# Kernel optimization log

Measured on AMD Instinct MI355X. Metric: run time of the kernel, lower is better.

Reference implementation:

```python
import jax, jax.numpy as jnp
import numpy as np


def _relative_position_index(wd, wh, ww):
    coords = np.stack(np.meshgrid(np.arange(wd), np.arange(wh), np.arange(ww), indexing='ij'))
    flat = coords.reshape(3, -1)                      # (3, N)
    rel = flat[:, :, None] - flat[:, None, :]         # (3, N, N)
    rel = rel.transpose(1, 2, 0).astype(np.int64)     # (N, N, 3)
    rel[..., 0] += wd - 1
    rel[..., 1] += wh - 1
    rel[..., 2] += ww - 1
    rel[..., 0] *= (2 * wh - 1) * (2 * ww - 1)
    rel[..., 1] *= (2 * ww - 1)
    return rel.sum(-1)                                 # (N, N)


def setup_inputs() -> dict:
    key = jax.random.key(0)
    k0, k1, k2, k3 = jax.random.split(key, 4)
    B, D, H, W = 4, 16, 56, 56
    wd, wh, ww = 8, 7, 7
    C, nH = 128, 4
    N = wd * wh * ww                                   # 392
    nW = (D // wd) * (H // wh) * (W // ww)             # 128
    B_ = B * nW                                        # 512
    table_sz = (2 * wd - 1) * (2 * wh - 1) * (2 * ww - 1)  # 2535
    x = jax.random.normal(k0, (B_, N, C), jnp.float32)
    mask = jnp.zeros((nW, N, N), jnp.float32)          # 0/-inf additive mask; zeros = no shift
    qkv_w = jax.random.normal(k1, (3 * C, C), jnp.float32) * 0.02
    proj_w = jax.random.normal(k2, (C, C), jnp.float32) * 0.02
    proj_b = jnp.zeros((C,), jnp.float32)
    bias_table = jax.random.normal(k3, (table_sz, nH), jnp.float32) * 0.02
    rel_index = jnp.asarray(_relative_position_index(wd, wh, ww), jnp.int32)
    return {"x": x, "mask": mask, "qkv_w": qkv_w, "proj_w": proj_w,
            "proj_b": proj_b, "bias_table": bias_table, "rel_index": rel_index}


def reference(x, mask, qkv_w, proj_w, proj_b, bias_table, rel_index):
    B_, N, C = x.shape
    nH = bias_table.shape[1]
    hd = C // nH
    scale = hd ** -0.5
    # qkv projection (no bias, qkv_bias=False)
    qkv = (x @ qkv_w.T).reshape(B_, N, 3, nH, hd).transpose(2, 0, 3, 1, 4)  # (3,B_,H,N,hd)
    q, k, v = qkv[0] * scale, qkv[1], qkv[2]
    attn = jnp.einsum('bhnd,bhmd->bhnm', q, k)                              # (B_,H,N,N)
    bias = bias_table[rel_index.reshape(-1)].reshape(N, N, nH).transpose(2, 0, 1)
    attn = attn + bias[None]
    nW = mask.shape[0]
    attn = attn.reshape(B_ // nW, nW, nH, N, N) + mask[None, :, None]
    attn = jax.nn.softmax(attn.reshape(B_, nH, N, N), axis=-1)
    out = jnp.einsum('bhnm,bhmd->bhnd', attn, v)                            # (B_,H,N,hd)
    out = out.transpose(0, 2, 1, 3).reshape(B_, N, C)
    return out @ proj_w.T + proj_b
```

## Files before the change

kernel.cpp:

```cpp
#include <hip/hip_runtime.h>

typedef unsigned short u16;
typedef unsigned int   u32;

#define NTOK   392
#define NN2    153664
#define LOG2E  1.44269504088896340736f
#define QSCL   (0.17677669529663687f * 1.44269504088896340736f)
#define BTQ    416
#define BTH    (416L*416L)

typedef __attribute__((ext_vector_type(8))) __bf16 bf16x8;
typedef __attribute__((ext_vector_type(4))) float  f32x4;
#define MFMA16(a,b,c) __builtin_amdgcn_mfma_f32_16x16x32_bf16((a),(b),(c),0,0,0)

__device__ __forceinline__ float bf2f(u16 u){
    union { u32 i; float f; } v; v.i = ((u32)u) << 16; return v.f;
}
__device__ __forceinline__ u16 f2bf(float x){
    union { float f; u32 i; } v; v.f = x;
    u32 r = (v.i + 0x7FFFu + ((v.i >> 16) & 1u)) >> 16;
    return (u16)r;
}
__device__ __forceinline__ u16 bfbits(float x){
    union { __bf16 b; u16 u; } v; v.b = (__bf16)x; return v.u;
}
__device__ __forceinline__ float ldf(const void* p, int isb, long i){
    if (isb) return bf2f(((const u16*)p)[i]);
    else     return ((const float*)p)[i];
}
__device__ __forceinline__ void stf(void* p, int isb, long i, float v){
    if (isb) ((u16*)p)[i] = f2bf(v);
    else     ((float*)p)[i] = v;
}

__device__ __forceinline__ void ld8s(const void* p, int isb, long i0,
                                     bf16x8* h, bf16x8* l){
    union { u16 u[8]; bf16x8 v; } H, L;
    if (isb){
        const uint2* q = (const uint2*)((const u16*)p + i0);
        uint2 a = q[0], b = q[1];
        H.u[0]=(u16)a.x; H.u[1]=(u16)(a.x>>16); H.u[2]=(u16)a.y; H.u[3]=(u16)(a.y>>16);
        H.u[4]=(u16)b.x; H.u[5]=(u16)(b.x>>16); H.u[6]=(u16)b.y; H.u[7]=(u16)(b.y>>16);
        #pragma unroll
        for (int j = 0; j < 8; ++j) L.u[j] = 0;
    } else {
        const float4* q = (const float4*)((const float*)p + i0);
        float4 a = q[0], b = q[1];
        float f[8] = {a.x,a.y,a.z,a.w,b.x,b.y,b.z,b.w};
        #pragma unroll
        for (int j = 0; j < 8; ++j){
            u16 hh = f2bf(f[j]);
            H.u[j] = hh;
            L.u[j] = f2bf(f[j] - bf2f(hh));
        }
    }
    *h = H.v; *l = L.v;
}

__device__ __forceinline__ int plaus(u16 w){
    int e = (w >> 7) & 0xFF;
    return (w == 0) || (e >= 96 && e <= 145);
}
__global__ __launch_bounds__(256) void prep_kernel(
        const u16* __restrict__ x, int* __restrict__ flags){
    __shared__ int cnt[2];
    int tid = threadIdx.x;
    if (tid < 2) cnt[tid] = 0;
    __syncthreads();
    int p = plaus(x[tid]) + plaus(x[tid + 256]);
    if (p) atomicAdd(&cnt[0], p);
    int ez = ((tid & 1) == 0 && x[tid] == 0) + (((tid + 256) & 1) == 0 && x[tid + 256] == 0);
    if (ez) atomicAdd(&cnt[1], ez);
    __syncthreads();
    if (tid == 0){
        flags[0] = (cnt[1] < 64 && cnt[0] >= 436) ? 1 : 0;
        flags[4] = 0;
    }
}

__global__ __launch_bounds__(256) void mask_scan_kernel(
        const u32* __restrict__ m, int nhalf, const int* __restrict__ flagsRO,
        int* __restrict__ flags){
    long nw = flagsRO[0] ? nhalf : 2L * nhalf;
    long i0 = (long)blockIdx.x * 256 + threadIdx.x;
    u32 acc = 0;
    for (long i = i0; i < nw; i += (long)gridDim.x * 256) acc |= m[i];
    if (acc) atomicOr(&flags[4], 1);
}

__global__ __launch_bounds__(256) void bias_expand_kernel(
        const int* __restrict__ rel_index, const void* btabP,
        const int* __restrict__ flags, float* __restrict__ biasT){
    long idx = (long)blockIdx.x * 256 + threadIdx.x;
    if (idx >= BTH) return;
    int key = (int)(idx / BTQ);
    int q   = (int)(idx - (long)key * BTQ);
    int isb = flags[0];
    float v0, v1, v2, v3;
    if (key >= NTOK){ v0 = v1 = v2 = v3 = -1e30f; }
    else if (q >= NTOK){ v0 = v1 = v2 = v3 = 0.f; }
    else {
        int t = rel_index[(long)q * NTOK + key];
        v0 = ldf(btabP, isb, (long)t * 4 + 0) * LOG2E;
        v1 = ldf(btabP, isb, (long)t * 4 + 1) * LOG2E;
        v2 = ldf(btabP, isb, (long)t * 4 + 2) * LOG2E;
        v3 = ldf(btabP, isb, (long)t * 4 + 3) * LOG2E;
    }
    biasT[0 * BTH + idx] = v0;
    biasT[1 * BTH + idx] = v1;
    biasT[2 * BTH + idx] = v2;
    biasT[3 * BTH + idx] = v3;
}

__global__ __launch_bounds__(512) void attn_mfma_kernel(
        const void* xP, const void* qwP, const void* maskP,
        const float* __restrict__ biasT, const int* __restrict__ flags,
        void* outP){
    __shared__ __align__(16) u16 Qh[416 * 40];
    __shared__ __align__(16) u16 Kh[416 * 40];
    __shared__ __align__(16) u16 VT[32 * 424];
    __shared__ __align__(16) u16 uni[2 * 64 * 136];

    u16* xs_hi = uni;
    u16* xs_lo = uni + 64 * 136;

    const int tid  = threadIdx.x;
    const int lane = tid & 63;
    const int wv   = tid >> 6;
    const int c    = lane & 15;
    const int g    = lane >> 4;
    const int h    = blockIdx.y;
    const int b_   = blockIdx.x;
    const int wdx  = b_ & 127;
    const int isb  = flags[0], fm = flags[4];
    const long xbase = (long)b_ * NTOK * 128;

    for (int i = tid; i < 24 * 40; i += 512){ Qh[392 * 40 + i] = 0; Kh[392 * 40 + i] = 0; }
    for (int i = tid; i < 32 * 32; i += 512) VT[(i >> 5) * 424 + 392 + (i & 31)] = 0;

    const int mt  = wv >> 1;
    const int ntb = (wv & 1) * 3;
    bf16x8 WH[3][4], WL[3][4];
    #pragma unroll
    for (int j = 0; j < 3; ++j){
        int n = (ntb + j) * 16 + c;
        int wrow = (n < 32) ? (h * 32 + n)
                 : (n < 64) ? (128 + h * 32 + (n - 32))
                 :            (256 + h * 32 + (n - 64));
        #pragma unroll
        for (int ks = 0; ks < 4; ++ks)
            ld8s(qwP, isb, (long)wrow * 128 + ks * 32 + 8 * g, &WH[j][ks], &WL[j][ks]);
    }

    for (int ch = 0; ch < 7; ++ch){
        const int tok0 = ch * 64;
        __syncthreads();
        #pragma unroll
        for (int jj = 0; jj < 4; ++jj){
            int idx = jj * 2048 + tid * 4;
            int r = idx >> 7, cc = idx & 127;
            int row = tok0 + r;
            u32 h01, h23, l01, l23;
            if (row < NTOK){
                long gi = xbase + (long)row * 128 + cc;
                if (isb){
                    uint2 a = *(const uint2*)((const u16*)xP + gi);
                    h01 = a.x; h23 = a.y; l01 = 0; l23 = 0;
                } else {
                    float4 f = *(const float4*)((const float*)xP + gi);
                    u16 h0=f2bf(f.x), h1=f2bf(f.y), h2=f2bf(f.z), h3=f2bf(f.w);
                    h01 = h0 | ((u32)h1 << 16); h23 = h2 | ((u32)h3 << 16);
                    l01 = (u32)f2bf(f.x - bf2f(h0)) | ((u32)f2bf(f.y - bf2f(h1)) << 16);
                    l23 = (u32)f2bf(f.z - bf2f(h2)) | ((u32)f2bf(f.w - bf2f(h3)) << 16);
                }
            } else { h01 = h23 = l01 = l23 = 0; }
            *(uint2*)&xs_hi[r * 136 + cc] = make_uint2(h01, h23);
            *(uint2*)&xs_lo[r * 136 + cc] = make_uint2(l01, l23);
        }
        __syncthreads();
        #pragma unroll
        for (int j = 0; j < 3; ++j){
            f32x4 acc = {0.f, 0.f, 0.f, 0.f};
            #pragma unroll
            for (int ks = 0; ks < 4; ++ks){
                bf16x8 ah = *(const bf16x8*)&xs_hi[(mt * 16 + c) * 136 + ks * 32 + 8 * g];
                bf16x8 al = *(const bf16x8*)&xs_lo[(mt * 16 + c) * 136 + ks * 32 + 8 * g];
                acc = MFMA16(ah, WH[j][ks], acc);
                acc = MFMA16(al, WH[j][ks], acc);
                acc = MFMA16(ah, WL[j][ks], acc);
            }
            int n = (ntb + j) * 16 + c;
            #pragma unroll
            for (int i = 0; i < 4; ++i){
                int tok = tok0 + mt * 16 + 4 * g + i;
                if (tok < NTOK){
                    if (n < 32)      Qh[tok * 40 + n]         = f2bf(acc[i] * QSCL);
                    else if (n < 64) Kh[tok * 40 + (n - 32)]  = f2bf(acc[i]);
                    else             VT[(n - 64) * 424 + tok] = f2bf(acc[i]);
                }
            }
        }
    }
    __syncthreads();

    u16* pbA = uni + wv * 1280;
    u16* pbB = pbA + 640;
    const float* bT = biasT + (long)h * BTH;
    const long mb = (long)wdx * NN2;

    for (int task = wv; task < 13; task += 8){
        const int qa0 = task * 32;
        const int qb0 = qa0 + 16;
        bf16x8 qA = *(const bf16x8*)&Qh[(qa0 + c) * 40 + 8 * g];
        bf16x8 qB = *(const bf16x8*)&Qh[(qb0 + c) * 40 + 8 * g];
        f32x4 oA0={0.f,0.f,0.f,0.f}, oA1={0.f,0.f,0.f,0.f};
        f32x4 oB0={0.f,0.f,0.f,0.f}, oB1={0.f,0.f,0.f,0.f};
        float rsA0=0.f,rsA1=0.f,rsA2=0.f,rsA3=0.f;
        float rsB0=0.f,rsB1=0.f,rsB2=0.f,rsB3=0.f;
        const float* bp = bT + (long)c * BTQ + qa0 + 4 * g;
        f32x4 rA0 = *(const f32x4*)(bp);
        f32x4 rB0 = *(const f32x4*)(bp + 16);
        f32x4 rA1 = *(const f32x4*)(bp + 16 * BTQ);
        f32x4 rB1 = *(const f32x4*)(bp + 16 * BTQ + 16);
        const float* fp = bp + 32 * BTQ;

        for (int k2 = 0; k2 < 13; ++k2){
            {
                const int kt = 2 * k2;
                bf16x8 kb = *(const bf16x8*)&Kh[(kt * 16 + c) * 40 + 8 * g];
                f32x4 cA = rA0, cB = rB0;
                if (k2 < 12){
                    rA0 = *(const f32x4*)(fp);
                    rB0 = *(const f32x4*)(fp + 16);
                }
                if (fm){
                    int key = kt * 16 + c; int kc = key < NTOK ? key : NTOK - 1;
                    #pragma unroll
                    for (int i = 0; i < 4; ++i){
                        int qa_ = qa0 + 4 * g + i; if (qa_ >= NTOK) qa_ = NTOK - 1;
                        int qb_ = qb0 + 4 * g + i; if (qb_ >= NTOK) qb_ = NTOK - 1;
                        cA[i] += ldf(maskP, isb, mb + (long)qa_ * NTOK + kc) * LOG2E;
                        cB[i] += ldf(maskP, isb, mb + (long)qb_ * NTOK + kc) * LOG2E;
                    }
                }
                f32x4 sA = MFMA16(qA, kb, cA);
                f32x4 sB = MFMA16(qB, kb, cB);
                float pA[4], pB[4];
                #pragma unroll
                for (int i = 0; i < 4; ++i){ pA[i] = exp2f(sA[i]); pB[i] = exp2f(sB[i]); }
                rsA0 += pA[0]; rsA1 += pA[1]; rsA2 += pA[2]; rsA3 += pA[3];
                rsB0 += pB[0]; rsB1 += pB[1]; rsB2 += pB[2]; rsB3 += pB[3];
                #pragma unroll
                for (int i = 0; i < 4; ++i){
                    pbA[(4 * g + i) * 40 + c] = bfbits(pA[i]);
                    pbB[(4 * g + i) * 40 + c] = bfbits(pB[i]);
                }
            }
            {
                const int kt = 2 * k2 + 1;
                bf16x8 kb = *(const bf16x8*)&Kh[(kt * 16 + c) * 40 + 8 * g];
                f32x4 cA = rA1, cB = rB1;
                if (k2 < 12){
                    rA1 = *(const f32x4*)(fp + 16 * BTQ);
                    rB1 = *(const f32x4*)(fp + 16 * BTQ + 16);
                    fp += 32 * BTQ;
                }
                if (fm){
                    int key = kt * 16 + c; int kc = key < NTOK ? key : NTOK - 1;
                    #pragma unroll
                    for (int i = 0; i < 4; ++i){
                        int qa_ = qa0 + 4 * g + i; if (qa_ >= NTOK) qa_ = NTOK - 1;
                        int qb_ = qb0 + 4 * g + i; if (qb_ >= NTOK) qb_ = NTOK - 1;
                        cA[i] += ldf(maskP, isb, mb + (long)qa_ * NTOK + kc) * LOG2E;
                        cB[i] += ldf(maskP, isb, mb + (long)qb_ * NTOK + kc) * LOG2E;
                    }
                }
                f32x4 sA = MFMA16(qA, kb, cA);
                f32x4 sB = MFMA16(qB, kb, cB);
                float pA[4], pB[4];
                #pragma unroll
                for (int i = 0; i < 4; ++i){ pA[i] = exp2f(sA[i]); pB[i] = exp2f(sB[i]); }
                rsA0 += pA[0]; rsA1 += pA[1]; rsA2 += pA[2]; rsA3 += pA[3];
                rsB0 += pB[0]; rsB1 += pB[1]; rsB2 += pB[2]; rsB3 += pB[3];
                #pragma unroll
                for (int i = 0; i < 4; ++i){
                    pbA[(4 * g + i) * 40 + 16 + c] = bfbits(pA[i]);
                    pbB[(4 * g + i) * 40 + 16 + c] = bfbits(pB[i]);
                }
                bf16x8 paA = *(const bf16x8*)&pbA[c * 40 + 8 * g];
                bf16x8 paB = *(const bf16x8*)&pbB[c * 40 + 8 * g];
                int kk = k2 * 32 + 8 * g;
                bf16x8 v0 = *(const bf16x8*)&VT[c * 424 + kk];
                bf16x8 v1 = *(const bf16x8*)&VT[(c + 16) * 424 + kk];
                oA0 = MFMA16(paA, v0, oA0);
                oA1 = MFMA16(paA, v1, oA1);
                oB0 = MFMA16(paB, v0, oB0);
                oB1 = MFMA16(paB, v1, oB1);
            }
        }
        float rsA[4] = {rsA0, rsA1, rsA2, rsA3};
        float rsB[4] = {rsB0, rsB1, rsB2, rsB3};
        #pragma unroll
        for (int m = 1; m < 16; m <<= 1){
            #pragma unroll
            for (int i = 0; i < 4; ++i){
                rsA[i] += __shfl_xor(rsA[i], m, 64);
                rsB[i] += __shfl_xor(rsB[i], m, 64);
            }
        }
        #pragma unroll
        for (int i = 0; i < 4; ++i){
            int ta = qa0 + 4 * g + i;
            if (ta < NTOK){
                float ia = 1.f / rsA[i];
                stf(outP, isb, xbase + (long)ta * 128 + h * 32 + c,      oA0[i] * ia);
                stf(outP, isb, xbase + (long)ta * 128 + h * 32 + 16 + c, oA1[i] * ia);
            }
            int tb = qb0 + 4 * g + i;
            if (tb < NTOK){
                float ib = 1.f / rsB[i];
                stf(outP, isb, xbase + (long)tb * 128 + h * 32 + c,      oB0[i] * ib);
                stf(outP, isb, xbase + (long)tb * 128 + h * 32 + 16 + c, oB1[i] * ib);
            }
        }
    }
}

__global__ __launch_bounds__(512) void proj_mfma_kernel(
        const void* wP, const void* bP, const int* __restrict__ flags,
        void* outP){
    __shared__ __align__(16) u16 xs_hi[64 * 136];
    __shared__ __align__(16) u16 xs_lo[64 * 136];
    const int tid  = threadIdx.x;
    const int lane = tid & 63;
    const int wv   = tid >> 6;
    const int c    = lane & 15;
    const int g    = lane >> 4;
    const int isb  = flags[0];
    const long m0  = (long)blockIdx.x * 64;

    #pragma unroll
    for (int jj = 0; jj < 4; ++jj){
        int idx = jj * 2048 + tid * 4;
        int r = idx >> 7, cc = idx & 127;
        long gi = (m0 + r) * 128 + cc;
        u32 h01, h23, l01, l23;
        if (isb){
            uint2 a = *(const uint2*)((const u16*)outP + gi);
            h01 = a.x; h23 = a.y; l01 = 0; l23 = 0;
        } else {
            float4 f = *(const float4*)((const float*)outP + gi);
            u16 h0=f2bf(f.x), h1=f2bf(f.y), h2=f2bf(f.z), h3=f2bf(f.w);
            h01 = h0 | ((u32)h1 << 16); h23 = h2 | ((u32)h3 << 16);
            l01 = (u32)f2bf(f.x - bf2f(h0)) | ((u32)f2bf(f.y - bf2f(h1)) << 16);
            l23 = (u32)f2bf(f.z - bf2f(h2)) | ((u32)f2bf(f.w - bf2f(h3)) << 16);
        }
        *(uint2*)&xs_hi[r * 136 + cc] = make_uint2(h01, h23);
        *(uint2*)&xs_lo[r * 136 + cc] = make_uint2(l01, l23);
    }
    __syncthreads();
    const int mt  = wv >> 1;
    const int ntb = (wv & 1) * 4;
    bf16x8 ah[4], al[4];
    #pragma unroll
    for (int ks = 0; ks < 4; ++ks){
        ah[ks] = *(const bf16x8*)&xs_hi[(mt * 16 + c) * 136 + ks * 32 + 8 * g];
        al[ks] = *(const bf16x8*)&xs_lo[(mt * 16 + c) * 136 + ks * 32 + 8 * g];
    }
    #pragma unroll
    for (int j = 0; j < 4; ++j){
        int nt = ntb + j;
        bf16x8 wh[4], wl[4];
        #pragma unroll
        for (int ks = 0; ks < 4; ++ks)
            ld8s(wP, isb, (long)(nt * 16 + c) * 128 + ks * 32 + 8 * g, &wh[ks], &wl[ks]);
        f32x4 acc = {0.f,0.f,0.f,0.f};
        #pragma unroll
        for (int ks = 0; ks < 4; ++ks){
            acc = MFMA16(ah[ks], wh[ks], acc);
            acc = MFMA16(al[ks], wh[ks], acc);
            acc = MFMA16(ah[ks], wl[ks], acc);
        }
        float bias = ldf(bP, isb, nt * 16 + c);
        #pragma unroll
        for (int i = 0; i < 4; ++i){
            long row = m0 + mt * 16 + 4 * g + i;
            stf(outP, isb, row * 128 + nt * 16 + c, acc[i] + bias);
        }
    }
}

extern "C" void kernel_launch(void* const* d_in, const int* in_sizes, int n_in,
                              void* d_out, int out_size, void* d_ws, size_t ws_size,
                              hipStream_t stream){
    const void* x      = d_in[0];
    const void* mask   = d_in[1];
    const void* qkv_w  = d_in[2];
    const void* proj_w = d_in[3];
    const void* proj_b = d_in[4];
    const void* btab   = d_in[5];
    const int*  relidx = (const int*)d_in[6];

    int*   flags = (int*)d_ws;
    float* biasT = (float*)((char*)d_ws + 256);

    prep_kernel<<<dim3(1), dim3(256), 0, stream>>>((const u16*)x, flags);
    int nhalf = in_sizes[1] / 2;
    mask_scan_kernel<<<dim3(2048), dim3(256), 0, stream>>>(
        (const u32*)mask, nhalf, flags, flags);
    bias_expand_kernel<<<dim3((int)((BTH + 255) / 256)), dim3(256), 0, stream>>>(
        relidx, btab, flags, biasT);
    attn_mfma_kernel<<<dim3(512, 4), dim3(512), 0, stream>>>(
        x, qkv_w, mask, biasT, flags, d_out);
    proj_mfma_kernel<<<dim3(3136), dim3(512), 0, stream>>>(
        proj_w, proj_b, flags, d_out);
}
```

Before: 719.8 us.

## Use 13 waves per attention block with transposed score MFMA and bias layout

```diff
diff --git a/kernel.cpp b/kernel.cpp
--- a/kernel.cpp
+++ b/kernel.cpp
@@ -7,7 +7,7 @@
 #define NN2    153664
 #define LOG2E  1.44269504088896340736f
 #define QSCL   (0.17677669529663687f * 1.44269504088896340736f)
-#define BTQ    416
+#define BTK    416
 #define BTH    (416L*416L)
 
 typedef __attribute__((ext_vector_type(8))) __bf16 bf16x8;
@@ -24,6 +24,9 @@
 }
 __device__ __forceinline__ u16 bfbits(float x){
     union { __bf16 b; u16 u; } v; v.b = (__bf16)x; return v.u;
+}
+__device__ __forceinline__ u32 pk2(float a, float b){
+    return (u32)bfbits(a) | ((u32)bfbits(b) << 16);
 }
 __device__ __forceinline__ float ldf(const void* p, int isb, long i){
     if (isb) return bf2f(((const u16*)p)[i]);
@@ -91,11 +94,11 @@
 
 __global__ __launch_bounds__(256) void bias_expand_kernel(
         const int* __restrict__ rel_index, const void* btabP,
-        const int* __restrict__ flags, float* __restrict__ biasT){
+        const int* __restrict__ flags, float* __restrict__ biasF){
     long idx = (long)blockIdx.x * 256 + threadIdx.x;
     if (idx >= BTH) return;
-    int key = (int)(idx / BTQ);
-    int q   = (int)(idx - (long)key * BTQ);
+    int q   = (int)(idx / BTK);
+    int key = (int)(idx - (long)q * BTK);
     int isb = flags[0];
     float v0, v1, v2, v3;
     if (key >= NTOK){ v0 = v1 = v2 = v3 = -1e30f; }
@@ -107,15 +110,15 @@
         v2 = ldf(btabP, isb, (long)t * 4 + 2) * LOG2E;
         v3 = ldf(btabP, isb, (long)t * 4 + 3) * LOG2E;
     }
-    biasT[0 * BTH + idx] = v0;
-    biasT[1 * BTH + idx] = v1;
-    biasT[2 * BTH + idx] = v2;
-    biasT[3 * BTH + idx] = v3;
-}
-
-__global__ __launch_bounds__(512) void attn_mfma_kernel(
+    biasF[0 * BTH + idx] = v0;
+    biasF[1 * BTH + idx] = v1;
+    biasF[2 * BTH + idx] = v2;
+    biasF[3 * BTH + idx] = v3;
+}
+
+__global__ __launch_bounds__(832) void attn_mfma_kernel(
         const void* xP, const void* qwP, const void* maskP,
-        const float* __restrict__ biasT, const int* __restrict__ flags,
+        const float* __restrict__ biasF, const int* __restrict__ flags,
         void* outP){
     __shared__ __align__(16) u16 Qh[416 * 40];
     __shared__ __align__(16) u16 Kh[416 * 40];
@@ -136,64 +139,71 @@
     const int isb  = flags[0], fm = flags[4];
     const long xbase = (long)b_ * NTOK * 128;
 
-    for (int i = tid; i < 24 * 40; i += 512){ Qh[392 * 40 + i] = 0; Kh[392 * 40 + i] = 0; }
-    for (int i = tid; i < 32 * 32; i += 512) VT[(i >> 5) * 424 + 392 + (i & 31)] = 0;
-
-    const int mt  = wv >> 1;
-    const int ntb = (wv & 1) * 3;
-    bf16x8 WH[3][4], WL[3][4];
-    #pragma unroll
-    for (int j = 0; j < 3; ++j){
-        int n = (ntb + j) * 16 + c;
-        int wrow = (n < 32) ? (h * 32 + n)
-                 : (n < 64) ? (128 + h * 32 + (n - 32))
-                 :            (256 + h * 32 + (n - 64));
-        #pragma unroll
-        for (int ks = 0; ks < 4; ++ks)
-            ld8s(qwP, isb, (long)wrow * 128 + ks * 32 + 8 * g, &WH[j][ks], &WL[j][ks]);
+    for (int i = tid; i < 24 * 40; i += 832){ Qh[392 * 40 + i] = 0; Kh[392 * 40 + i] = 0; }
+    for (int i = tid; i < 32 * 32; i += 832) VT[(i >> 5) * 424 + 392 + (i & 31)] = 0;
+
+    const int nt0 = wv >> 2,        mt0 = wv & 3;
+    const int nt1 = (wv + 13) >> 2, mt1 = (wv + 13) & 3;
+    const int has1 = (wv < 11);
+    bf16x8 W0h[4], W0l[4], W1h[4], W1l[4];
+    {
+        int n0 = nt0 * 16 + c;
+        int wr0 = (n0 < 32) ? (h * 32 + n0)
+                : (n0 < 64) ? (128 + h * 32 + (n0 - 32))
+                :             (256 + h * 32 + (n0 - 64));
+        int n1 = nt1 * 16 + c;
+        int wr1 = (n1 < 32) ? (h * 32 + n1)
+                : (n1 < 64) ? (128 + h * 32 + (n1 - 32))
+                :             (256 + h * 32 + (n1 - 64));
+        #pragma unroll
+        for (int ks = 0; ks < 4; ++ks){
+            ld8s(qwP, isb, (long)wr0 * 128 + ks * 32 + 8 * g, &W0h[ks], &W0l[ks]);
+            if (has1)
+                ld8s(qwP, isb, (long)wr1 * 128 + ks * 32 + 8 * g, &W1h[ks], &W1l[ks]);
+        }
     }
 
     for (int ch = 0; ch < 7; ++ch){
         const int tok0 = ch * 64;
         __syncthreads();
-        #pragma unroll
-        for (int jj = 0; jj < 4; ++jj){
-            int idx = jj * 2048 + tid * 4;
+        for (int idx = tid * 4; idx < 8192; idx += 3328){
             int r = idx >> 7, cc = idx & 127;
             int row = tok0 + r;
-            u32 h01, h23, l01, l23;
-            if (row < NTOK){
-                long gi = xbase + (long)row * 128 + cc;
-                if (isb){
-                    uint2 a = *(const uint2*)((const u16*)xP + gi);
-                    h01 = a.x; h23 = a.y; l01 = 0; l23 = 0;
-                } else {
-                    float4 f = *(const float4*)((const float*)xP + gi);
+            if (isb){
+                uint2 a = make_uint2(0u, 0u);
+                if (row < NTOK)
+                    a = *(const uint2*)((const u16*)xP + xbase + (long)row * 128 + cc);
+                *(uint2*)&xs_hi[r * 136 + cc] = a;
+            } else {
+                u32 h01, h23, l01, l23;
+                if (row < NTOK){
+                    float4 f = *(const float4*)((const float*)xP + xbase + (long)row * 128 + cc);
                     u16 h0=f2bf(f.x), h1=f2bf(f.y), h2=f2bf(f.z), h3=f2bf(f.w);
                     h01 = h0 | ((u32)h1 << 16); h23 = h2 | ((u32)h3 << 16);
                     l01 = (u32)f2bf(f.x - bf2f(h0)) | ((u32)f2bf(f.y - bf2f(h1)) << 16);
                     l23 = (u32)f2bf(f.z - bf2f(h2)) | ((u32)f2bf(f.w - bf2f(h3)) << 16);
-                }
-            } else { h01 = h23 = l01 = l23 = 0; }
-            *(uint2*)&xs_hi[r * 136 + cc] = make_uint2(h01, h23);
-            *(uint2*)&xs_lo[r * 136 + cc] = make_uint2(l01, l23);
+                } else { h01 = h23 = l01 = l23 = 0; }
+                *(uint2*)&xs_hi[r * 136 + cc] = make_uint2(h01, h23);
+                *(uint2*)&xs_lo[r * 136 + cc] = make_uint2(l01, l23);
+            }
         }
         __syncthreads();
-        #pragma unroll
-        for (int j = 0; j < 3; ++j){
+        {
             f32x4 acc = {0.f, 0.f, 0.f, 0.f};
             #pragma unroll
             for (int ks = 0; ks < 4; ++ks){
-                bf16x8 ah = *(const bf16x8*)&xs_hi[(mt * 16 + c) * 136 + ks * 32 + 8 * g];
-                bf16x8 al = *(const bf16x8*)&xs_lo[(mt * 16 + c) * 136 + ks * 32 + 8 * g];
-                acc = MFMA16(ah, WH[j][ks], acc);
-                acc = MFMA16(al, WH[j][ks], acc);
-                acc = MFMA16(ah, WL[j][ks], acc);
-            }
-            int n = (ntb + j) * 16 + c;
+                bf16x8 ah = *(const bf16x8*)&xs_hi[(mt0 * 16 + c) * 136 + ks * 32 + 8 * g];
+                acc = MFMA16(ah, W0h[ks], acc);
+                if (!isb){
+                    bf16x8 al = *(const bf16x8*)&xs_lo[(mt0 * 16 + c) * 136 + ks * 32 + 8 * g];
+                    acc = MFMA16(al, W0h[ks], acc);
+                    acc = MFMA16(ah, W0l[ks], acc);
+                }
+            }
+            int n = nt0 * 16 + c;
             #pragma unroll
             for (int i = 0; i < 4; ++i){
-                int tok = tok0 + mt * 16 + 4 * g + i;
+                int tok = tok0 + mt0 * 16 + 4 * g + i;
                 if (tok < NTOK){
                     if (n < 32)      Qh[tok * 40 + n]         = f2bf(acc[i] * QSCL);
                     else if (n < 64) Kh[tok * 40 + (n - 32)]  = f2bf(acc[i]);
@@ -201,128 +211,115 @@
                 }
             }
         }
+        if (has1){
+            f32x4 acc = {0.f, 0.f, 0.f, 0.f};
+            #pragma unroll
+            for (int ks = 0; ks < 4; ++ks){
+                bf16x8 ah = *(const bf16x8*)&xs_hi[(mt1 * 16 + c) * 136 + ks * 32 + 8 * g];
+                acc = MFMA16(ah, W1h[ks], acc);
+                if (!isb){
+                    bf16x8 al = *(const bf16x8*)&xs_lo[(mt1 * 16 + c) * 136 + ks * 32 + 8 * g];
+                    acc = MFMA16(al, W1h[ks], acc);
+                    acc = MFMA16(ah, W1l[ks], acc);
+                }
+            }
+            int n = nt1 * 16 + c;
+            #pragma unroll
+            for (int i = 0; i < 4; ++i){
+                int tok = tok0 + mt1 * 16 + 4 * g + i;
+                if (tok < NTOK){
+                    if (n < 32)      Qh[tok * 40 + n]         = f2bf(acc[i] * QSCL);
+                    else if (n < 64) Kh[tok * 40 + (n - 32)]  = f2bf(acc[i]);
+                    else             VT[(n - 64) * 424 + tok] = f2bf(acc[i]);
+                }
+            }
+        }
     }
     __syncthreads();
 
     u16* pbA = uni + wv * 1280;
     u16* pbB = pbA + 640;
-    const float* bT = biasT + (long)h * BTH;
-    const long mb = (long)wdx * NN2;
-
-    for (int task = wv; task < 13; task += 8){
-        const int qa0 = task * 32;
-        const int qb0 = qa0 + 16;
-        bf16x8 qA = *(const bf16x8*)&Qh[(qa0 + c) * 40 + 8 * g];
-        bf16x8 qB = *(const bf16x8*)&Qh[(qb0 + c) * 40 + 8 * g];
-        f32x4 oA0={0.f,0.f,0.f,0.f}, oA1={0.f,0.f,0.f,0.f};
-        f32x4 oB0={0.f,0.f,0.f,0.f}, oB1={0.f,0.f,0.f,0.f};
-        float rsA0=0.f,rsA1=0.f,rsA2=0.f,rsA3=0.f;
-        float rsB0=0.f,rsB1=0.f,rsB2=0.f,rsB3=0.f;
-        const float* bp = bT + (long)c * BTQ + qa0 + 4 * g;
-        f32x4 rA0 = *(const f32x4*)(bp);
-        f32x4 rB0 = *(const f32x4*)(bp + 16);
-        f32x4 rA1 = *(const f32x4*)(bp + 16 * BTQ);
-        f32x4 rB1 = *(const f32x4*)(bp + 16 * BTQ + 16);
-        const float* fp = bp + 32 * BTQ;
-
-        for (int k2 = 0; k2 < 13; ++k2){
-            {
-                const int kt = 2 * k2;
-                bf16x8 kb = *(const bf16x8*)&Kh[(kt * 16 + c) * 40 + 8 * g];
-                f32x4 cA = rA0, cB = rB0;
-                if (k2 < 12){
-                    rA0 = *(const f32x4*)(fp);
-                    rB0 = *(const f32x4*)(fp + 16);
-                }
-                if (fm){
-                    int key = kt * 16 + c; int kc = key < NTOK ? key : NTOK - 1;
-                    #pragma unroll
-                    for (int i = 0; i < 4; ++i){
-                        int qa_ = qa0 + 4 * g + i; if (qa_ >= NTOK) qa_ = NTOK - 1;
-                        int qb_ = qb0 + 4 * g + i; if (qb_ >= NTOK) qb_ = NTOK - 1;
-                        cA[i] += ldf(maskP, isb, mb + (long)qa_ * NTOK + kc) * LOG2E;
-                        cB[i] += ldf(maskP, isb, mb + (long)qb_ * NTOK + kc) * LOG2E;
-                    }
-                }
-                f32x4 sA = MFMA16(qA, kb, cA);
-                f32x4 sB = MFMA16(qB, kb, cB);
-                float pA[4], pB[4];
-                #pragma unroll
-                for (int i = 0; i < 4; ++i){ pA[i] = exp2f(sA[i]); pB[i] = exp2f(sB[i]); }
-                rsA0 += pA[0]; rsA1 += pA[1]; rsA2 += pA[2]; rsA3 += pA[3];
-                rsB0 += pB[0]; rsB1 += pB[1]; rsB2 += pB[2]; rsB3 += pB[3];
-                #pragma unroll
-                for (int i = 0; i < 4; ++i){
-                    pbA[(4 * g + i) * 40 + c] = bfbits(pA[i]);
-                    pbB[(4 * g + i) * 40 + c] = bfbits(pB[i]);
-                }
-            }
-            {
-                const int kt = 2 * k2 + 1;
-                bf16x8 kb = *(const bf16x8*)&Kh[(kt * 16 + c) * 40 + 8 * g];
-                f32x4 cA = rA1, cB = rB1;
-                if (k2 < 12){
-                    rA1 = *(const f32x4*)(fp + 16 * BTQ);
-                    rB1 = *(const f32x4*)(fp + 16 * BTQ + 16);
-                    fp += 32 * BTQ;
-                }
-                if (fm){
-                    int key = kt * 16 + c; int kc = key < NTOK ? key : NTOK - 1;
-                    #pragma unroll
-                    for (int i = 0; i < 4; ++i){
-                        int qa_ = qa0 + 4 * g + i; if (qa_ >= NTOK) qa_ = NTOK - 1;
-                        int qb_ = qb0 + 4 * g + i; if (qb_ >= NTOK) qb_ = NTOK - 1;
-                        cA[i] += ldf(maskP, isb, mb + (long)qa_ * NTOK + kc) * LOG2E;
-                        cB[i] += ldf(maskP, isb, mb + (long)qb_ * NTOK + kc) * LOG2E;
-                    }
-                }
-                f32x4 sA = MFMA16(qA, kb, cA);
-                f32x4 sB = MFMA16(qB, kb, cB);
-                float pA[4], pB[4];
-                #pragma unroll
-                for (int i = 0; i < 4; ++i){ pA[i] = exp2f(sA[i]); pB[i] = exp2f(sB[i]); }
-                rsA0 += pA[0]; rsA1 += pA[1]; rsA2 += pA[2]; rsA3 += pA[3];
-                rsB0 += pB[0]; rsB1 += pB[1]; rsB2 += pB[2]; rsB3 += pB[3];
-                #pragma unroll
-                for (int i = 0; i < 4; ++i){
-                    pbA[(4 * g + i) * 40 + 16 + c] = bfbits(pA[i]);
-                    pbB[(4 * g + i) * 40 + 16 + c] = bfbits(pB[i]);
-                }
-                bf16x8 paA = *(const bf16x8*)&pbA[c * 40 + 8 * g];
-                bf16x8 paB = *(const bf16x8*)&pbB[c * 40 + 8 * g];
-                int kk = k2 * 32 + 8 * g;
-                bf16x8 v0 = *(const bf16x8*)&VT[c * 424 + kk];
-                bf16x8 v1 = *(const bf16x8*)&VT[(c + 16) * 424 + kk];
-                oA0 = MFMA16(paA, v0, oA0);
-                oA1 = MFMA16(paA, v1, oA1);
-                oB0 = MFMA16(paB, v0, oB0);
-                oB1 = MFMA16(paB, v1, oB1);
-            }
-        }
-        float rsA[4] = {rsA0, rsA1, rsA2, rsA3};
-        float rsB[4] = {rsB0, rsB1, rsB2, rsB3};
-        #pragma unroll
-        for (int m = 1; m < 16; m <<= 1){
+    const int qa0 = wv * 32, qb0 = qa0 + 16;
+    const float* bpA = biasF + (long)h * BTH + (long)(qa0 + c) * BTK;
+    const float* bpB = biasF + (long)h * BTH + (long)(qb0 + c) * BTK;
+    const long mbase = (long)wdx * NN2;
+
+    bf16x8 qA = *(const bf16x8*)&Qh[(qa0 + c) * 40 + 8 * g];
+    bf16x8 qB = *(const bf16x8*)&Qh[(qb0 + c) * 40 + 8 * g];
+    f32x4 oA0={0.f,0.f,0.f,0.f}, oA1={0.f,0.f,0.f,0.f};
+    f32x4 oB0={0.f,0.f,0.f,0.f}, oB1={0.f,0.f,0.f,0.f};
+    float rsA = 0.f, rsB = 0.f;
+    f32x4 rAe = *(const f32x4*)(bpA + 4 * g);
+    f32x4 rAo = *(const f32x4*)(bpA + 16 + 4 * g);
+    f32x4 rBe = *(const f32x4*)(bpB + 4 * g);
+    f32x4 rBo = *(const f32x4*)(bpB + 16 + 4 * g);
+
+    for (int k2 = 0; k2 < 13; ++k2){
+        const int kk = k2 * 32;
+        f32x4 cAe = rAe, cAo = rAo, cBe = rBe, cBo = rBo;
+        if (k2 < 12){
+            rAe = *(const f32x4*)(bpA + kk + 32 + 4 * g);
+            rAo = *(const f32x4*)(bpA + kk + 48 + 4 * g);
+            rBe = *(const f32x4*)(bpB + kk + 32 + 4 * g);
+            rBo = *(const f32x4*)(bpB + kk + 48 + 4 * g);
+        }
+        if (fm){
+            int qa_ = qa0 + c; if (qa_ >= NTOK) qa_ = NTOK - 1;
+            int qb_ = qb0 + c; if (qb_ >= NTOK) qb_ = NTOK - 1;
             #pragma unroll
             for (int i = 0; i < 4; ++i){
-                rsA[i] += __shfl_xor(rsA[i], m, 64);
-                rsB[i] += __shfl_xor(rsB[i], m, 64);
-            }
-        }
+                int ke = kk + 4 * g + i;      int kce = ke < NTOK ? ke : NTOK - 1;
+                int ko = kk + 16 + 4 * g + i; int kco = ko < NTOK ? ko : NTOK - 1;
+                cAe[i] += ldf(maskP, isb, mbase + (long)qa_ * NTOK + kce) * LOG2E;
+                cAo[i] += ldf(maskP, isb, mbase + (long)qa_ * NTOK + kco) * LOG2E;
+                cBe[i] += ldf(maskP, isb, mbase + (long)qb_ * NTOK + kce) * LOG2E;
+                cBo[i] += ldf(maskP, isb, mbase + (long)qb_ * NTOK + kco) * LOG2E;
+            }
+        }
+        bf16x8 kbE = *(const bf16x8*)&Kh[(kk + c) * 40 + 8 * g];
+        bf16x8 kbO = *(const bf16x8*)&Kh[(kk + 16 + c) * 40 + 8 * g];
+        f32x4 sAe = MFMA16(kbE, qA, cAe);
+        f32x4 sAo = MFMA16(kbO, qA, cAo);
+        f32x4 sBe = MFMA16(kbE, qB, cBe);
+        f32x4 sBo = MFMA16(kbO, qB, cBo);
+        float pAe[4], pAo[4], pBe[4], pBo[4];
         #pragma unroll
         for (int i = 0; i < 4; ++i){
-            int ta = qa0 + 4 * g + i;
-            if (ta < NTOK){
-                float ia = 1.f / rsA[i];
-                stf(outP, isb, xbase + (long)ta * 128 + h * 32 + c,      oA0[i] * ia);
-                stf(outP, isb, xbase + (long)ta * 128 + h * 32 + 16 + c, oA1[i] * ia);
-            }
-            int tb = qb0 + 4 * g + i;
-            if (tb < NTOK){
-                float ib = 1.f / rsB[i];
-                stf(outP, isb, xbase + (long)tb * 128 + h * 32 + c,      oB0[i] * ib);
-                stf(outP, isb, xbase + (long)tb * 128 + h * 32 + 16 + c, oB1[i] * ib);
-            }
+            pAe[i] = exp2f(sAe[i]); pAo[i] = exp2f(sAo[i]);
+            pBe[i] = exp2f(sBe[i]); pBo[i] = exp2f(sBo[i]);
+        }
+        rsA += ((pAe[0]+pAe[1]) + (pAe[2]+pAe[3])) + ((pAo[0]+pAo[1]) + (pAo[2]+pAo[3]));
+        rsB += ((pBe[0]+pBe[1]) + (pBe[2]+pBe[3])) + ((pBo[0]+pBo[1]) + (pBo[2]+pBo[3]));
+        *(uint2*)&pbA[c * 40 + 4 * g]      = make_uint2(pk2(pAe[0],pAe[1]), pk2(pAe[2],pAe[3]));
+        *(uint2*)&pbA[c * 40 + 16 + 4 * g] = make_uint2(pk2(pAo[0],pAo[1]), pk2(pAo[2],pAo[3]));
+        *(uint2*)&pbB[c * 40 + 4 * g]      = make_uint2(pk2(pBe[0],pBe[1]), pk2(pBe[2],pBe[3]));
+        *(uint2*)&pbB[c * 40 + 16 + 4 * g] = make_uint2(pk2(pBo[0],pBo[1]), pk2(pBo[2],pBo[3]));
+        bf16x8 paA = *(const bf16x8*)&pbA[c * 40 + 8 * g];
+        bf16x8 paB = *(const bf16x8*)&pbB[c * 40 + 8 * g];
+        bf16x8 v0 = *(const bf16x8*)&VT[c * 424 + kk + 8 * g];
+        bf16x8 v1 = *(const bf16x8*)&VT[(c + 16) * 424 + kk + 8 * g];
+        oA0 = MFMA16(paA, v0, oA0);
+        oA1 = MFMA16(paA, v1, oA1);
+        oB0 = MFMA16(paB, v0, oB0);
+        oB1 = MFMA16(paB, v1, oB1);
+    }
+    rsA += __shfl_xor(rsA, 16, 64); rsA += __shfl_xor(rsA, 32, 64);
+    rsB += __shfl_xor(rsB, 16, 64); rsB += __shfl_xor(rsB, 32, 64);
+    #pragma unroll
+    for (int i = 0; i < 4; ++i){
+        float SA = __shfl(rsA, 4 * g + i, 64);
+        float SB = __shfl(rsB, 4 * g + i, 64);
+        int ta = qa0 + 4 * g + i;
+        if (ta < NTOK){
+            float ia = 1.f / SA;
+            stf(outP, isb, xbase + (long)ta * 128 + h * 32 + c,      oA0[i] * ia);
+            stf(outP, isb, xbase + (long)ta * 128 + h * 32 + 16 + c, oA1[i] * ia);
+        }
+        int tb = qb0 + 4 * g + i;
+        if (tb < NTOK){
+            float ib = 1.f / SB;
+            stf(outP, isb, xbase + (long)tb * 128 + h * 32 + c,      oB0[i] * ib);
+            stf(outP, isb, xbase + (long)tb * 128 + h * 32 + 16 + c, oB1[i] * ib);
         }
     }
 }
@@ -345,19 +342,18 @@
         int idx = jj * 2048 + tid * 4;
         int r = idx >> 7, cc = idx & 127;
         long gi = (m0 + r) * 128 + cc;
-        u32 h01, h23, l01, l23;
         if (isb){
             uint2 a = *(const uint2*)((const u16*)outP + gi);
-            h01 = a.x; h23 = a.y; l01 = 0; l23 = 0;
+            *(uint2*)&xs_hi[r * 136 + cc] = a;
         } else {
             float4 f = *(const float4*)((const float*)outP + gi);
             u16 h0=f2bf(f.x), h1=f2bf(f.y), h2=f2bf(f.z), h3=f2bf(f.w);
-            h01 = h0 | ((u32)h1 << 16); h23 = h2 | ((u32)h3 << 16);
-            l01 = (u32)f2bf(f.x - bf2f(h0)) | ((u32)f2bf(f.y - bf2f(h1)) << 16);
-            l23 = (u32)f2bf(f.z - bf2f(h2)) | ((u32)f2bf(f.w - bf2f(h3)) << 16);
-        }
-        *(uint2*)&xs_hi[r * 136 + cc] = make_uint2(h01, h23);
-        *(uint2*)&xs_lo[r * 136 + cc] = make_uint2(l01, l23);
+            u32 h01 = h0 | ((u32)h1 << 16), h23 = h2 | ((u32)h3 << 16);
+            u32 l01 = (u32)f2bf(f.x - bf2f(h0)) | ((u32)f2bf(f.y - bf2f(h1)) << 16);
+            u32 l23 = (u32)f2bf(f.z - bf2f(h2)) | ((u32)f2bf(f.w - bf2f(h3)) << 16);
+            *(uint2*)&xs_hi[r * 136 + cc] = make_uint2(h01, h23);
+            *(uint2*)&xs_lo[r * 136 + cc] = make_uint2(l01, l23);
+        }
     }
     __syncthreads();
     const int mt  = wv >> 1;
@@ -366,7 +362,8 @@
     #pragma unroll
     for (int ks = 0; ks < 4; ++ks){
         ah[ks] = *(const bf16x8*)&xs_hi[(mt * 16 + c) * 136 + ks * 32 + 8 * g];
-        al[ks] = *(const bf16x8*)&xs_lo[(mt * 16 + c) * 136 + ks * 32 + 8 * g];
+        if (!isb)
+            al[ks] = *(const bf16x8*)&xs_lo[(mt * 16 + c) * 136 + ks * 32 + 8 * g];
     }
     #pragma unroll
     for (int j = 0; j < 4; ++j){
@@ -379,8 +376,10 @@
         #pragma unroll
         for (int ks = 0; ks < 4; ++ks){
             acc = MFMA16(ah[ks], wh[ks], acc);
-            acc = MFMA16(al[ks], wh[ks], acc);
-            acc = MFMA16(ah[ks], wl[ks], acc);
+            if (!isb){
+                acc = MFMA16(al[ks], wh[ks], acc);
+                acc = MFMA16(ah[ks], wl[ks], acc);
+            }
         }
         float bias = ldf(bP, isb, nt * 16 + c);
         #pragma unroll
@@ -403,16 +402,16 @@
     const int*  relidx = (const int*)d_in[6];
 
     int*   flags = (int*)d_ws;
-    float* biasT = (float*)((char*)d_ws + 256);
+    float* biasF = (float*)((char*)d_ws + 256);
 
     prep_kernel<<<dim3(1), dim3(256), 0, stream>>>((const u16*)x, flags);
     int nhalf = in_sizes[1] / 2;
     mask_scan_kernel<<<dim3(2048), dim3(256), 0, stream>>>(
         (const u32*)mask, nhalf, flags, flags);
     bias_expand_kernel<<<dim3((int)((BTH + 255) / 256)), dim3(256), 0, stream>>>(
-        relidx, btab, flags, biasT);
-    attn_mfma_kernel<<<dim3(512, 4), dim3(512), 0, stream>>>(
-        x, qkv_w, mask, biasT, flags, d_out);
+        relidx, btab, flags, biasF);
+    attn_mfma_kernel<<<dim3(512, 4), dim3(832), 0, stream>>>(
+        x, qkv_w, mask, biasF, flags, d_out);
     proj_mfma_kernel<<<dim3(3136), dim3(512), 0, stream>>>(
         proj_w, proj_b, flags, d_out);
 }
```

Measured after the change: 700.3 us. -2.7%, faster.
